# Performance work log

Hardware: AMD Instinct MI355X
Metric: run time of the kernel (lower is better)

The kernel has to match this reference:

```python
import jax, jax.numpy as jnp
import numpy as np

H = W = 64          # input_resolution
C = 256             # dim
HEADS = 8
WS = 8              # window_size
SHIFT = WS // 2
DEPTH = 2           # block 0: no shift, block 1: shifted + mask
HIDDEN = 4 * C      # mlp_ratio * dim
B = 8
N = WS * WS                 # tokens per window
NW = (H // WS) * (W // WS)  # windows per image
EPS = 1e-5


def _rel_pos_index():
    coords = np.stack(np.meshgrid(np.arange(WS), np.arange(WS), indexing='ij')).reshape(2, -1)
    rel = (coords[:, :, None] - coords[:, None, :]).transpose(1, 2, 0)
    rel[:, :, 0] += WS - 1
    rel[:, :, 1] += WS - 1
    rel[:, :, 0] *= 2 * WS - 1
    return rel.sum(-1)  # [N, N] indices into (2*ws-1)^2 table

REL_IDX = jnp.asarray(_rel_pos_index())


def _attn_mask():
    # Swin shift mask: label 3x3 regions, compare window-token labels
    img = np.zeros((H, W))
    slices = (slice(0, -WS), slice(-WS, -SHIFT), slice(-SHIFT, None))
    cnt = 0
    for hs in slices:
        for ws_ in slices:
            img[hs, ws_] = cnt
            cnt += 1
    mw = img.reshape(H // WS, WS, W // WS, WS).transpose(0, 2, 1, 3).reshape(-1, N)
    diff = mw[:, None, :] - mw[:, :, None]
    return jnp.asarray(np.where(diff != 0, -100.0, 0.0), dtype=np.float32)  # [nW, N, N]

ATTN_MASK = _attn_mask()


def layernorm(x, g, b):
    mu = jnp.mean(x, axis=-1, keepdims=True)
    var = jnp.mean((x - mu) ** 2, axis=-1, keepdims=True)
    return (x - mu) * jax.lax.rsqrt(var + EPS) * g + b


def setup_inputs() -> dict:
    key = jax.random.key(0)
    ks = jax.random.split(key, 6)
    s = 0.02
    return {
        'x': jax.random.normal(ks[0], (B, H * W, C), jnp.float32),
        'qkv_w': jax.random.normal(ks[1], (DEPTH, C, 3 * C), jnp.float32) * s,
        'qkv_b': jnp.zeros((DEPTH, 3 * C), jnp.float32),
        'proj_w': jax.random.normal(ks[2], (DEPTH, C, C), jnp.float32) * s,
        'proj_b': jnp.zeros((DEPTH, C), jnp.float32),
        'ln1_g': jnp.ones((DEPTH, C), jnp.float32),
        'ln1_b': jnp.zeros((DEPTH, C), jnp.float32),
        'ln2_g': jnp.ones((DEPTH, C), jnp.float32),
        'ln2_b': jnp.zeros((DEPTH, C), jnp.float32),
        'fc1_w': jax.random.normal(ks[3], (DEPTH, C, HIDDEN), jnp.float32) * s,
        'fc1_b': jnp.zeros((DEPTH, HIDDEN), jnp.float32),
        'fc2_w': jax.random.normal(ks[4], (DEPTH, HIDDEN, C), jnp.float32) * s,
        'fc2_b': jnp.zeros((DEPTH, C), jnp.float32),
        'rpb': jax.random.normal(ks[5], (DEPTH, (2 * WS - 1) ** 2, HEADS), jnp.float32) * s,
    }


def window_attention(xw, qw, qb, pw, pb, rpb_i, mask):
    # xw: [B*nW, N, C]
    B_ = xw.shape[0]
    d = C // HEADS
    qkv = (xw @ qw + qb).reshape(B_, N, 3, HEADS, d).transpose(2, 0, 3, 1, 4)
    q, k, v = qkv[0] * (d ** -0.5), qkv[1], qkv[2]   # [B_, h, N, d]
    attn = jnp.einsum('bhnd,bhmd->bhnm', q, k)
    bias = rpb_i[REL_IDX.reshape(-1)].reshape(N, N, HEADS).transpose(2, 0, 1)
    attn = attn + bias[None]
    if mask is not None:
        attn = attn.reshape(-1, NW, HEADS, N, N) + mask[None, :, None]
        attn = attn.reshape(-1, HEADS, N, N)
    attn = jax.nn.softmax(attn, axis=-1)
    out = jnp.einsum('bhnm,bhmd->bhnd', attn, v).transpose(0, 2, 1, 3).reshape(B_, N, C)
    return out @ pw + pb


def reference(x, qkv_w, qkv_b, proj_w, proj_b, ln1_g, ln1_b, ln2_g, ln2_b,
              fc1_w, fc1_b, fc2_w, fc2_b, rpb):
    for i in range(DEPTH):
        shift = 0 if i % 2 == 0 else SHIFT
        mask = None if shift == 0 else ATTN_MASK
        shortcut = x
        h = layernorm(x, ln1_g[i], ln1_b[i]).reshape(-1, H, W, C)
        if shift:
            h = jnp.roll(h, (-shift, -shift), axis=(1, 2))
        # window partition -> [B*nW, N, C]
        hw = h.reshape(-1, H // WS, WS, W // WS, WS, C).transpose(0, 1, 3, 2, 4, 5).reshape(-1, N, C)
        aw = window_attention(hw, qkv_w[i], qkv_b[i], proj_w[i], proj_b[i], rpb[i], mask)
        # window reverse
        h = aw.reshape(-1, H // WS, W // WS, WS, WS, C).transpose(0, 1, 3, 2, 4, 5).reshape(-1, H, W, C)
        if shift:
            h = jnp.roll(h, (shift, shift), axis=(1, 2))
        x = shortcut + h.reshape(-1, H * W, C)
        m = layernorm(x, ln2_g[i], ln2_b[i])
        m = jax.nn.gelu(m @ fc1_w[i] + fc1_b[i], approximate=False) @ fc2_w[i] + fc2_b[i]
        x = x + m
    return x
```

## Files before the change

### kernel.cpp

```cpp
#include <hip/hip_runtime.h>
#include <hip/hip_bf16.h>


typedef __hip_bfloat16 bf16;
typedef unsigned short u16;
typedef unsigned int u32;
typedef short short8 __attribute__((ext_vector_type(8)));
typedef float floatx4 __attribute__((ext_vector_type(4)));

#define DEVI static __device__ __forceinline__
#define WAITCNT_VM(n) asm volatile("s_waitcnt vmcnt(" #n ")" ::: "memory")

DEVI float lo16(u32 u) { union { u32 i; float f; } x; x.i = u << 16; return x.f; }
DEVI float hi16(u32 u) { union { u32 i; float f; } x; x.i = u & 0xffff0000u; return x.f; }
DEVI float b2f(u16 u) { union { u32 i; float f; } x; x.i = ((u32)u) << 16; return x.f; }
DEVI u16 f2b(float f) {
  union { float f; u32 i; } x; x.f = f;
  u32 r = x.i + 0x7fffu + ((x.i >> 16) & 1u);
  return (u16)(r >> 16);
}
DEVI float in_elem(const void* p, size_t i, int m) {
  return m ? b2f(((const u16*)p)[i]) : ((const float*)p)[i];
}
DEVI int swlab(int g) { return (g < 56) ? 0 : (g < 60 ? 1 : 2); }

DEVI float gelu_cheap(float v) {
  const float u = v * v;
  const float t = v * __builtin_fmaf(0.1029436f, u, 2.3022090f);
  const float e = __builtin_amdgcn_exp2f(t);
  const float r = __builtin_amdgcn_rcpf(e + 1.0f);
  return __builtin_fmaf(-v, r, v);
}

DEVI void async16(const bf16* g, bf16* l) {
  __builtin_amdgcn_global_load_lds((const __attribute__((address_space(1))) u32*)g,
                                   (__attribute__((address_space(3))) u32*)l, 16, 0, 0);
}

__global__ void k_detect(const u32* __restrict__ ln1g, int* __restrict__ mode) {
  if (threadIdx.x == 0 && blockIdx.x == 0)
    *mode = (ln1g[0] == 0x3F803F80u) ? 1 : 0;
}

__global__ __launch_bounds__(256) void k_ingest_ln(const void* __restrict__ xin,
    float* __restrict__ xf, const void* __restrict__ gamw, const void* __restrict__ betw,
    bf16* __restrict__ outp, const int* __restrict__ mode)
{
  const int m = *mode;
  const int l = threadIdx.x & 63, w = threadIdx.x >> 6;
  const int row = blockIdx.x * 4 + w;
  const int t = row & 63, win = row >> 6;
  const int bb = win >> 6, wi = win & 63;
  const int gh = ((wi >> 3) << 3) + (t >> 3);
  const int gw = ((wi & 7) << 3) + (t & 7);
  const int srow = (bb << 12) + (gh << 6) + gw;
  const int cb = l << 2;
  float4 v;
  if (m) {
    const uint2 u = *(const uint2*)((const u16*)xin + (size_t)srow * 256 + cb);
    v = make_float4(lo16(u.x), hi16(u.x), lo16(u.y), hi16(u.y));
  } else {
    v = ((const float4*)((const float*)xin + (size_t)srow * 256))[l];
  }
  ((float4*)(xf + (size_t)srow * 256))[l] = v;
  float s = v.x + v.y + v.z + v.w;
#pragma unroll
  for (int off = 32; off > 0; off >>= 1) s += __shfl_xor(s, off, 64);
  const float mu = s * 0.00390625f;
  const float a = v.x - mu, b = v.y - mu, c = v.z - mu, d = v.w - mu;
  float q = a * a + b * b + c * c + d * d;
#pragma unroll
  for (int off = 32; off > 0; off >>= 1) q += __shfl_xor(q, off, 64);
  const float rs = rsqrtf(q * 0.00390625f + 1e-5f);
  const float o0 = a * rs * in_elem(gamw, cb + 0, m) + in_elem(betw, cb + 0, m);
  const float o1 = b * rs * in_elem(gamw, cb + 1, m) + in_elem(betw, cb + 1, m);
  const float o2 = c * rs * in_elem(gamw, cb + 2, m) + in_elem(betw, cb + 2, m);
  const float o3 = d * rs * in_elem(gamw, cb + 3, m) + in_elem(betw, cb + 3, m);
  const u32 p0 = (u32)f2b(o0) | ((u32)f2b(o1) << 16);
  const u32 p1 = (u32)f2b(o2) | ((u32)f2b(o3) << 16);
  *(uint2*)((u16*)outp + (size_t)row * 256 + cb) = make_uint2(p0, p1);
}

__global__ __launch_bounds__(256) void k_transpose(
    const void* __restrict__ src, bf16* __restrict__ dst,
    const int* __restrict__ mode, int estride, int dstride, int R, int Cn) {
  __shared__ float T[32][33];
  const int m = *mode;
  const int tx = threadIdx.x & 31, ty = threadIdx.x >> 5;
  const int bc = blockIdx.x << 5, br = blockIdx.y << 5;
  for (int d = 0; d < 2; ++d) {
    __syncthreads();
#pragma unroll
    for (int dy = 0; dy < 4; ++dy) {
      const int r = br + ty + dy * 8;
      T[ty + dy * 8][tx] = in_elem(src, (size_t)d * estride + (size_t)r * Cn + bc + tx, m);
    }
    __syncthreads();
#pragma unroll
    for (int dy = 0; dy < 4; ++dy) {
      const int c = bc + ty + dy * 8;
      ((u16*)dst)[(size_t)d * dstride + (size_t)c * R + br + tx] = f2b(T[tx][ty + dy * 8]);
    }
  }
}

template <int EPI>
__global__ __launch_bounds__(256, 3) void k_gemm(
    const bf16* __restrict__ A, const bf16* __restrict__ Bt,
    const void* __restrict__ bias, bf16* __restrict__ outb,
    const int* __restrict__ mode, int boff, int K, int N)
{
  __shared__ __align__(16) bf16 As[3][128 * 32];
  __shared__ __align__(16) bf16 Bs[3][128 * 32];
  __shared__ __align__(16) float EPs[4][4][72];
  const int md = *mode;
  const int tid = threadIdx.x;
  const int l = tid & 63, wid = tid >> 6;
  const int wr = wid >> 1, wc = wid & 1;

  const int gx = gridDim.x;
  const int nwg = gx * gridDim.y;
  int fid = blockIdx.y * gx + blockIdx.x;
  if (!(nwg & 7)) fid = (fid & 7) * (nwg >> 3) + (fid >> 3);
  const int row0 = (fid / gx) * 128;
  const int col0 = (fid % gx) * 128;

  const int lrow = l >> 2;
  const int lkof = (((l & 3) ^ ((l >> 3) & 3)) * 8);
  const int qsw  = (((l >> 4) ^ ((l >> 1) & 3)) * 8);

  floatx4 acc[4][4];
#pragma unroll
  for (int mi = 0; mi < 4; ++mi)
#pragma unroll
    for (int ni = 0; ni < 4; ++ni)
      acc[mi][ni] = (floatx4){0.f, 0.f, 0.f, 0.f};

  auto stage = [&](int b, int kbase) {
    const int kk = kbase + lkof;
#pragma unroll
    for (int c = 0; c < 2; ++c) {
      const int seg = c * 4 + wid;
      async16(A + (size_t)(row0 + seg * 16 + lrow) * K + kk, &As[b][seg * 512]);
      async16(Bt + (size_t)(col0 + seg * 16 + lrow) * K + kk, &Bs[b][seg * 512]);
    }
  };

  const int nsl = K >> 5;
  stage(0, 0);
  stage(1, 32);

  for (int s = 0; s < nsl; ++s) {
    const int cur = s % 3;
    if (s < nsl - 1) { WAITCNT_VM(4); }
    else            { WAITCNT_VM(0); }
    __builtin_amdgcn_s_barrier();
    if (s + 2 < nsl) stage((s + 2) % 3, (s + 2) * 32);

    short8 af[4], bq[4];
#pragma unroll
    for (int mi = 0; mi < 4; ++mi)
      af[mi] = *(const short8*)&As[cur][(wr * 64 + mi * 16 + (l & 15)) * 32 + qsw];
#pragma unroll
    for (int ni = 0; ni < 4; ++ni)
      bq[ni] = *(const short8*)&Bs[cur][(wc * 64 + ni * 16 + (l & 15)) * 32 + qsw];
#pragma unroll
    for (int mi = 0; mi < 4; ++mi)
#pragma unroll
      for (int ni = 0; ni < 4; ++ni)
        acc[mi][ni] = __builtin_amdgcn_mfma_f32_16x16x32_bf16(af[mi], bq[ni], acc[mi][ni], 0, 0, 0);
  }

  float* EPw = &EPs[wid][0][0];
  const int cl = l & 15, rq = l >> 4;
  const int colb = wc * 64 + cl * 4;
  float bias4[4];
#pragma unroll
  for (int i = 0; i < 4; ++i) bias4[i] = in_elem(bias, (size_t)boff + col0 + colb + i, md);

#pragma unroll
  for (int mi = 0; mi < 4; ++mi) {
#pragma unroll
    for (int r = 0; r < 4; ++r) {
#pragma unroll
      for (int ni = 0; ni < 4; ++ni)
        EPw[rq * 72 + ni * 16 + cl] = acc[mi][ni][r];
      const float4 av = *(const float4*)&EPw[rq * 72 + cl * 4];
      float v0 = av.x + bias4[0], v1 = av.y + bias4[1];
      float v2 = av.z + bias4[2], v3 = av.w + bias4[3];
      if (EPI == 1) {
        v0 = gelu_cheap(v0); v1 = gelu_cheap(v1);
        v2 = gelu_cheap(v2); v3 = gelu_cheap(v3);
      }
      const int row = row0 + wr * 64 + mi * 16 + rq * 4 + r;
      const u32 p0 = (u32)f2b(v0) | ((u32)f2b(v1) << 16);
      const u32 p1 = (u32)f2b(v2) | ((u32)f2b(v3) << 16);
      *(uint2*)((u16*)outb + (size_t)row * N + col0 + colb) = make_uint2(p0, p1);
    }
  }
}

template <int MODE>
__global__ __launch_bounds__(256, 2) void k_fullN(
    const bf16* __restrict__ A, const bf16* __restrict__ Bt,
    const void* __restrict__ bias, const void* __restrict__ lng,
    const void* __restrict__ lnb, void* __restrict__ outp,
    float* __restrict__ xf, const int* __restrict__ mode,
    int boff, int lnoff, int K, int shift)
{
  __shared__ __align__(16) char smem[61440];
  bf16* As = (bf16*)smem;
  bf16* Bs = (bf16*)(smem + 12288);
  const int md = *mode;
  const int tid = threadIdx.x;
  const int l = tid & 63, w = tid >> 6;

  int fid = blockIdx.x;
  const int nwg = gridDim.x;
  if (!(nwg & 7)) fid = (fid & 7) * (nwg >> 3) + (fid >> 3);
  const int row0 = fid * 64;

  const int lrow = l >> 2;
  const int lkof = (((l & 3) ^ ((l >> 3) & 3)) * 8);
  const int qsw  = (((l >> 4) ^ ((l >> 1) & 3)) * 8);

  floatx4 acc[16];
#pragma unroll
  for (int ni = 0; ni < 16; ++ni) acc[ni] = (floatx4){0.f, 0.f, 0.f, 0.f};

  auto stage = [&](int b, int kbase) {
    const int kk = kbase + lkof;
    async16(A + (size_t)(row0 + w * 16 + lrow) * K + kk, As + b * 2048 + w * 512);
#pragma unroll
    for (int c = 0; c < 4; ++c) {
      const int seg = c * 4 + w;
      async16(Bt + (size_t)(seg * 16 + lrow) * K + kk, Bs + b * 8192 + seg * 512);
    }
  };

  const int nsl = K >> 5;
  stage(0, 0);
  stage(1, 32);

  for (int s = 0; s < nsl; ++s) {
    const int cur = s % 3;
    if (s < nsl - 1) { WAITCNT_VM(5); }
    else            { WAITCNT_VM(0); }
    __builtin_amdgcn_s_barrier();
    if (s + 2 < nsl) stage((s + 2) % 3, (s + 2) * 32);

    const short8 af = *(const short8*)&As[cur * 2048 + (w * 16 + (l & 15)) * 32 + qsw];
#pragma unroll
    for (int ni = 0; ni < 16; ++ni) {
      const short8 bq = *(const short8*)&Bs[cur * 8192 + (ni * 16 + (l & 15)) * 32 + qsw];
      acc[ni] = __builtin_amdgcn_mfma_f32_16x16x32_bf16(af, bq, acc[ni], 0, 0, 0);
    }
  }

  __syncthreads();

  float* EPw = (float*)smem + w * 1088;
  const int cl = l & 15, rq = l >> 4;
  const int c4 = l * 4;

  float bias4[4], g4[4], b4[4];
#pragma unroll
  for (int i = 0; i < 4; ++i) bias4[i] = in_elem(bias, (size_t)boff + c4 + i, md);
#pragma unroll
  for (int i = 0; i < 4; ++i) {
    g4[i] = in_elem(lng, (size_t)lnoff + c4 + i, md);
    b4[i] = in_elem(lnb, (size_t)lnoff + c4 + i, md);
  }

  for (int r = 0; r < 4; ++r) {
#pragma unroll
    for (int ni = 0; ni < 16; ++ni)
      EPw[rq * 272 + ni * 16 + cl] = acc[ni][r];

#pragma unroll
    for (int g = 0; g < 4; ++g) {
      const int lrow_g = row0 + w * 16 + g * 4 + r;
      const float4 av = *(const float4*)&EPw[g * 272 + c4];

      const int t_ = lrow_g & 63, win = lrow_g >> 6;
      const int bb = win >> 6, wi2 = win & 63;
      int gh = ((wi2 >> 3) << 3) + (t_ >> 3);
      int gw = ((wi2 & 7) << 3) + (t_ & 7);
      gh = (gh + shift) & 63; gw = (gw + shift) & 63;
      const int resrow = (bb << 12) + (gh << 6) + gw;
      const int dstrow = resrow;

      const float4 xv = *(const float4*)(xf + (size_t)resrow * 256 + c4);
      float t0 = av.x + bias4[0] + xv.x;
      float t1 = av.y + bias4[1] + xv.y;
      float t2 = av.z + bias4[2] + xv.z;
      float t3 = av.w + bias4[3] + xv.w;

      float s = t0 + t1 + t2 + t3;
#pragma unroll
      for (int off = 32; off > 0; off >>= 1) s += __shfl_xor(s, off, 64);
      const float mu = s * 0.00390625f;
      const float d0 = t0 - mu, d1 = t1 - mu, d2 = t2 - mu, d3 = t3 - mu;
      float q = d0 * d0 + d1 * d1 + d2 * d2 + d3 * d3;
#pragma unroll
      for (int off = 32; off > 0; off >>= 1) q += __shfl_xor(q, off, 64);
      const float rs = rsqrtf(q * 0.00390625f + 1e-5f);

      *(float4*)(xf + (size_t)resrow * 256 + c4) = make_float4(t0, t1, t2, t3);
      const u32 p0 = (u32)f2b(d0 * rs * g4[0] + b4[0]) | ((u32)f2b(d1 * rs * g4[1] + b4[1]) << 16);
      const u32 p1 = (u32)f2b(d2 * rs * g4[2] + b4[2]) | ((u32)f2b(d3 * rs * g4[3] + b4[3]) << 16);
      *(uint2*)((u16*)outp + (size_t)dstrow * 256 + c4) = make_uint2(p0, p1);
    }
  }
}

template <int MODE>
__global__ __launch_bounds__(512, 2) void k_mlp(
    const bf16* __restrict__ A, const bf16* __restrict__ W1t, const bf16* __restrict__ W2t,
    const void* __restrict__ b1, const void* __restrict__ b2,
    const void* __restrict__ lng, const void* __restrict__ lnb,
    void* __restrict__ outp, float* __restrict__ xf, const int* __restrict__ mode,
    int b1off, int b2off, int lnoff)
{
  __shared__ __align__(16) char smem[163840];
  bf16* Al = (bf16*)smem;
  bf16* Wl = (bf16*)(smem + 65536);
  u16*  Hl = (u16*)(smem + 131072);
  const int md = *mode;
  const int tid = threadIdx.x;
  const int l = tid & 63, w = tid >> 6;
  const int rh = w >> 2, wq = w & 3;
  int fid = blockIdx.x;
  const int nwg = gridDim.x;
  if (!(nwg & 7)) fid = (fid & 7) * (nwg >> 3) + (fid >> 3);
  const int row0 = fid * 128;

  const int lr4 = l >> 2;
  const int lkof = (((l & 3) ^ ((l >> 3) & 3)) * 8);
  const int qsw  = (((l >> 4) ^ ((l >> 1) & 3)) * 8);
  const int cl = l & 15, rq = l >> 4;

  floatx4 acc2[4][4];
#pragma unroll
  for (int mi = 0; mi < 4; ++mi)
#pragma unroll
    for (int ni = 0; ni < 4; ++ni)
      acc2[mi][ni] = (floatx4){0.f, 0.f, 0.f, 0.f};

  auto stageW1 = [&](int c, int s, int b) {
    const size_t gr = (size_t)(c * 128 + w * 16 + lr4) * 256;
#pragma unroll
    for (int ss = 0; ss < 4; ++ss)
      async16(W1t + gr + (s + ss) * 32 + lkof, Wl + b * 16384 + ss * 4096 + w * 512);
  };
  auto stageW2 = [&](int c, int q, int b) {
#pragma unroll
    for (int qq = 0; qq < 2; ++qq)
#pragma unroll
      for (int cc = 0; cc < 2; ++cc) {
        const int seg = w * 2 + cc;
        async16(W2t + (size_t)(seg * 16 + lr4) * 1024 + c * 128 + (q + qq) * 32 + lkof,
                Wl + b * 16384 + qq * 8192 + seg * 512);
      }
  };
  auto stage_g = [&](int g) {
    const int c = g >> 2, sub = g & 3, b = g & 1;
    if (sub < 2) stageW1(c, 4 * sub, b);
    else         stageW2(c, 2 * (sub - 2), b);
  };

#pragma unroll
  for (int s = 0; s < 8; ++s)
    async16(A + (size_t)(row0 + w * 16 + lr4) * 256 + s * 32 + lkof, Al + s * 4096 + w * 512);
  stage_g(0);

  int ph = 0;
  for (int c = 0; c < 8; ++c) {
    floatx4 acc1[4][2];
#pragma unroll
    for (int mi = 0; mi < 4; ++mi)
#pragma unroll
      for (int bni = 0; bni < 2; ++bni)
        acc1[mi][bni] = (floatx4){0.f, 0.f, 0.f, 0.f};

    for (int p = 0; p < 2; ++p, ++ph) {
      WAITCNT_VM(0);
      __builtin_amdgcn_s_barrier();
      if (ph + 1 < 32) stage_g(ph + 1);
      const int buf = ph & 1;
#pragma unroll
      for (int h2 = 0; h2 < 4; ++h2) {
        const int ks = 4 * p + h2;
        short8 af[4];
#pragma unroll
        for (int mi = 0; mi < 4; ++mi)
          af[mi] = *(const short8*)&Al[ks * 4096 + (rh * 64 + mi * 16 + cl) * 32 + qsw];
#pragma unroll
        for (int bni = 0; bni < 2; ++bni) {
          const short8 bq = *(const short8*)(Wl + buf * 16384 + h2 * 4096 +
                                             (wq * 32 + bni * 16 + cl) * 32 + qsw);
#pragma unroll
          for (int mi = 0; mi < 4; ++mi)
            acc1[mi][bni] = __builtin_amdgcn_mfma_f32_16x16x32_bf16(af[mi], bq, acc1[mi][bni], 0, 0, 0);
        }
      }
    }

#pragma unroll
    for (int bni = 0; bni < 2; ++bni) {
      const int h32 = bni * 16 + cl;
      const float bv = in_elem(b1, (size_t)b1off + c * 128 + wq * 32 + h32, md);
      const int hq = h32 >> 3, he = h32 & 7;
#pragma unroll
      for (int mi = 0; mi < 4; ++mi)
#pragma unroll
        for (int r = 0; r < 4; ++r) {
          const int hr = rh * 64 + mi * 16 + rq * 4 + r;
          Hl[wq * 4096 + hr * 32 + ((hq ^ ((hr >> 1) & 3)) * 8) + he] =
              f2b(gelu_cheap(acc1[mi][bni][r] + bv));
        }
    }
    asm volatile("s_waitcnt lgkmcnt(0)" ::: "memory");

    for (int p = 0; p < 2; ++p, ++ph) {
      WAITCNT_VM(0);
      __builtin_amdgcn_s_barrier();
      if (ph + 1 < 32) stage_g(ph + 1);
      const int buf = ph & 1;
#pragma unroll
      for (int qq = 0; qq < 2; ++qq) {
        const int q2 = 2 * p + qq;
        short8 hf[4];
#pragma unroll
        for (int mi = 0; mi < 4; ++mi)
          hf[mi] = *(const short8*)((const bf16*)&Hl[q2 * 4096 + (rh * 64 + mi * 16 + cl) * 32 + qsw]);
#pragma unroll
        for (int ni = 0; ni < 4; ++ni) {
          const short8 bq = *(const short8*)(Wl + buf * 16384 + qq * 8192 +
                                             (wq * 64 + ni * 16 + cl) * 32 + qsw);
#pragma unroll
          for (int mi = 0; mi < 4; ++mi)
            acc2[mi][ni] = __builtin_amdgcn_mfma_f32_16x16x32_bf16(hf[mi], bq, acc2[mi][ni], 0, 0, 0);
        }
      }
    }
  }

  __syncthreads();
  float* EPf = (float*)smem;
#pragma unroll
  for (int mi = 0; mi < 4; ++mi)
#pragma unroll
    for (int ni = 0; ni < 4; ++ni)
#pragma unroll
      for (int r = 0; r < 4; ++r)
        EPf[(rh * 64 + mi * 16 + rq * 4 + r) * 272 + wq * 64 + ni * 16 + cl] = acc2[mi][ni][r];
  __syncthreads();

  const int c4 = l * 4;
  float bias4[4], g4[4], b4[4];
#pragma unroll
  for (int i = 0; i < 4; ++i) bias4[i] = in_elem(b2, (size_t)b2off + c4 + i, md);
  if (MODE == 1) {
#pragma unroll
    for (int i = 0; i < 4; ++i) {
      g4[i] = in_elem(lng, (size_t)lnoff + c4 + i, md);
      b4[i] = in_elem(lnb, (size_t)lnoff + c4 + i, md);
    }
  }

  for (int rr = 0; rr < 16; ++rr) {
    const int lrow_g = row0 + w * 16 + rr;
    const float4 av = *(const float4*)&EPf[(w * 16 + rr) * 272 + c4];
    const float4 xv = *(const float4*)(xf + (size_t)lrow_g * 256 + c4);
    float t0 = av.x + bias4[0] + xv.x;
    float t1 = av.y + bias4[1] + xv.y;
    float t2 = av.z + bias4[2] + xv.z;
    float t3 = av.w + bias4[3] + xv.w;

    if (MODE == 2) {
      *(float4*)((float*)outp + (size_t)lrow_g * 256 + c4) = make_float4(t0, t1, t2, t3);
      continue;
    }

    const int bb = lrow_g >> 12, th = (lrow_g >> 6) & 63, tw = lrow_g & 63;
    const int gh = (th + 60) & 63, gw = (tw + 60) & 63;
    const int wi2 = ((gh >> 3) << 3) + (gw >> 3);
    const int tt = ((gh & 7) << 3) + (gw & 7);
    const int dstrow = (bb << 12) + (wi2 << 6) + tt;

    float s = t0 + t1 + t2 + t3;
#pragma unroll
    for (int off = 32; off > 0; off >>= 1) s += __shfl_xor(s, off, 64);
    const float mu = s * 0.00390625f;
    const float d0 = t0 - mu, d1 = t1 - mu, d2 = t2 - mu, d3 = t3 - mu;
    float q = d0 * d0 + d1 * d1 + d2 * d2 + d3 * d3;
#pragma unroll
    for (int off = 32; off > 0; off >>= 1) q += __shfl_xor(q, off, 64);
    const float rs = rsqrtf(q * 0.00390625f + 1e-5f);

    *(float4*)(xf + (size_t)lrow_g * 256 + c4) = make_float4(t0, t1, t2, t3);
    const u32 p0 = (u32)f2b(d0 * rs * g4[0] + b4[0]) | ((u32)f2b(d1 * rs * g4[1] + b4[1]) << 16);
    const u32 p1 = (u32)f2b(d2 * rs * g4[2] + b4[2]) | ((u32)f2b(d3 * rs * g4[3] + b4[3]) << 16);
    *(uint2*)((u16*)outp + (size_t)dstrow * 256 + c4) = make_uint2(p0, p1);
  }
}

__global__ __launch_bounds__(256, 2) void k_attn(
    const bf16* __restrict__ qkv, const void* __restrict__ rpb,
    bf16* __restrict__ outp, const int* __restrict__ mode, int eoff, int shifted)
{
  __shared__ __align__(16) u16 Pl[4][64][72];
  __shared__ __align__(16) u16 Vt[4][32][72];
  __shared__ float rpbs[4][228];
  const int md = *mode;
  const int l = threadIdx.x & 63, w = threadIdx.x >> 6;
  const int cl = l & 15, qd = l >> 4;
  const int ko = qd * 8;
  const int win = blockIdx.x;
  const int wi = win & 63;
  const int whb = (wi >> 3) << 3, wwb = (wi & 7) << 3;
  const size_t rowbase = (size_t)win * 64 * 768;

  for (int hh = 0; hh < 2; ++hh) {
    const int h = w + hh * 4;
    for (int i = l; i < 225; i += 64)
      rpbs[w][i] = in_elem(rpb, (size_t)eoff + (size_t)i * 8 + h, md);
    {
      const u16* vrow = (const u16*)(qkv + rowbase + (size_t)l * 768 + 512 + h * 32);
#pragma unroll
      for (int n = 0; n < 32; ++n) Vt[w][n][l] = vrow[n];
    }
    short8 qf[4], kf[4];
#pragma unroll
    for (int t = 0; t < 4; ++t) {
      qf[t] = *(const short8*)(qkv + rowbase + (size_t)(t * 16 + cl) * 768 + h * 32 + ko);
      kf[t] = *(const short8*)(qkv + rowbase + (size_t)(t * 16 + cl) * 768 + 256 + h * 32 + ko);
    }
    __syncthreads();

    floatx4 S[4][4];
#pragma unroll
    for (int mi = 0; mi < 4; ++mi)
#pragma unroll
      for (int ni = 0; ni < 4; ++ni)
        S[mi][ni] = __builtin_amdgcn_mfma_f32_16x16x32_bf16(qf[mi], kf[ni], (floatx4){0.f, 0.f, 0.f, 0.f}, 0, 0, 0);

    int cty[4], ctx[4], clab[4];
#pragma unroll
    for (int ni = 0; ni < 4; ++ni) {
      const int ct = ni * 16 + cl;
      cty[ni] = ct >> 3; ctx[ni] = ct & 7;
      clab[ni] = shifted ? (swlab(whb + cty[ni]) * 3 + swlab(wwb + ctx[ni])) : 0;
    }

    float invs[4][4];
#pragma unroll
    for (int mi = 0; mi < 4; ++mi) {
#pragma unroll
      for (int r = 0; r < 4; ++r) {
        const int rt = mi * 16 + qd * 4 + r;
        const int rty = rt >> 3, rtx = rt & 7;
        const int rlab = shifted ? (swlab(whb + rty) * 3 + swlab(wwb + rtx)) : 0;
        float sv[4];
#pragma unroll
        for (int ni = 0; ni < 4; ++ni) {
          float x = S[mi][ni][r] * 0.17677669529663687f;
          x += rpbs[w][(rty - cty[ni] + 7) * 15 + (rtx - ctx[ni] + 7)];
          if (shifted && (rlab != clab[ni])) x -= 100.f;
          sv[ni] = x;
        }
        float mx = fmaxf(fmaxf(sv[0], sv[1]), fmaxf(sv[2], sv[3]));
        mx = fmaxf(mx, __shfl_xor(mx, 1, 64));
        mx = fmaxf(mx, __shfl_xor(mx, 2, 64));
        mx = fmaxf(mx, __shfl_xor(mx, 4, 64));
        mx = fmaxf(mx, __shfl_xor(mx, 8, 64));
        float sum = 0.f;
#pragma unroll
        for (int ni = 0; ni < 4; ++ni) { sv[ni] = __expf(sv[ni] - mx); sum += sv[ni]; }
        sum += __shfl_xor(sum, 1, 64);
        sum += __shfl_xor(sum, 2, 64);
        sum += __shfl_xor(sum, 4, 64);
        sum += __shfl_xor(sum, 8, 64);
        invs[mi][r] = __builtin_amdgcn_rcpf(sum);
#pragma unroll
        for (int ni = 0; ni < 4; ++ni) Pl[w][rt][ni * 16 + cl] = f2b(sv[ni]);
      }
    }
    __syncthreads();

    floatx4 O[4][2];
#pragma unroll
    for (int mi = 0; mi < 4; ++mi)
#pragma unroll
      for (int nv = 0; nv < 2; ++nv)
        O[mi][nv] = (floatx4){0.f, 0.f, 0.f, 0.f};
    short8 vf[2][2];
#pragma unroll
    for (int nv = 0; nv < 2; ++nv)
#pragma unroll
      for (int kk = 0; kk < 2; ++kk)
        vf[nv][kk] = *(const short8*)&Vt[w][nv * 16 + cl][kk * 32 + ko];
#pragma unroll
    for (int mi = 0; mi < 4; ++mi) {
      const short8 pf0 = *(const short8*)&Pl[w][mi * 16 + cl][ko];
      const short8 pf1 = *(const short8*)&Pl[w][mi * 16 + cl][32 + ko];
#pragma unroll
      for (int nv = 0; nv < 2; ++nv) {
        O[mi][nv] = __builtin_amdgcn_mfma_f32_16x16x32_bf16(pf0, vf[nv][0], O[mi][nv], 0, 0, 0);
        O[mi][nv] = __builtin_amdgcn_mfma_f32_16x16x32_bf16(pf1, vf[nv][1], O[mi][nv], 0, 0, 0);
      }
    }

#pragma unroll
    for (int mi = 0; mi < 4; ++mi)
#pragma unroll
      for (int nv = 0; nv < 2; ++nv)
#pragma unroll
        for (int r = 0; r < 4; ++r) {
          const int row = mi * 16 + qd * 4 + r;
          ((u16*)outp)[((size_t)win * 64 + row) * 256 + h * 32 + nv * 16 + cl] =
              f2b(O[mi][nv][r] * invs[mi][r]);
        }
    __syncthreads();
  }
}

extern "C" void kernel_launch(void* const* d_in, const int* in_sizes, int n_in,
                              void* d_out, int out_size, void* d_ws, size_t ws_size,
                              hipStream_t stream) {
  (void)in_sizes; (void)n_in; (void)out_size; (void)ws_size;
  const void* x_in   = d_in[0];
  const void* qkv_w  = d_in[1];
  const void* qkv_b  = d_in[2];
  const void* proj_w = d_in[3];
  const void* proj_b = d_in[4];
  const void* ln1_g  = d_in[5];
  const void* ln1_b  = d_in[6];
  const void* ln2_g  = d_in[7];
  const void* ln2_b  = d_in[8];
  const void* fc1_w  = d_in[9];
  const void* fc1_b  = d_in[10];
  const void* fc2_w  = d_in[11];
  const void* fc2_b  = d_in[12];
  const void* rpb    = d_in[13];

  char* ws = (char*)d_ws;
  float* xf  = (float*)ws;
  bf16* bufQ = (bf16*)(ws + 100663296);
  bf16* bufB = (bf16*)(ws + 150994944);
  bf16* wT   = (bf16*)(ws + 167772160);
  int* mode  = (int*)(ws + 170917888);

  k_detect<<<1, 1, 0, stream>>>((const u32*)ln1_g, mode);
  k_ingest_ln<<<8192, 256, 0, stream>>>(x_in, xf, ln1_g, ln1_b, bufB, mode);

  k_transpose<<<dim3(24, 8), 256, 0, stream>>>(qkv_w,  wT,          mode, 196608, 786432, 256, 768);
  k_transpose<<<dim3(8, 8), 256, 0, stream>>>(proj_w, wT + 196608, mode, 65536, 786432, 256, 256);
  k_transpose<<<dim3(32, 8), 256, 0, stream>>>(fc1_w, wT + 262144, mode, 262144, 786432, 256, 1024);
  k_transpose<<<dim3(8, 32), 256, 0, stream>>>(fc2_w, wT + 524288, mode, 262144, 786432, 1024, 256);

  for (int i = 0; i < 2; ++i) {
    const int shift = i ? 4 : 0;
    bf16* base  = wT + (size_t)i * 786432;
    bf16* qkvT  = base;
    bf16* projT = base + 196608;
    bf16* fc1T  = base + 262144;
    bf16* fc2T  = base + 524288;

    k_gemm<0><<<dim3(6, 256), 256, 0, stream>>>(bufB, qkvT, qkv_b, bufQ, mode, i * 768, 256, 768);
    k_attn<<<512, 256, 0, stream>>>(bufQ, rpb, bufB, mode, i * 1800, i);
    k_fullN<0><<<512, 256, 0, stream>>>(bufB, projT, proj_b, ln2_g, ln2_b, bufQ, xf, mode,
                                        i * 256, i * 256, 256, shift);
    if (i == 0)
      k_mlp<1><<<256, 512, 0, stream>>>(bufQ, fc1T, fc2T, fc1_b, fc2_b, ln1_g, ln1_b,
                                        bufB, xf, mode, 0, 0, 256);
    else
      k_mlp<2><<<256, 512, 0, stream>>>(bufQ, fc1T, fc2T, fc1_b, fc2_b, nullptr, nullptr,
                                        d_out, xf, mode, 1024, 256, 0);
  }
}
```

Before: 388.8 us.

## Precompute bias+mask table, vectorize V staging, drop per-wave barriers in attention

```diff
diff --git a/kernel.cpp b/kernel.cpp
--- a/kernel.cpp
+++ b/kernel.cpp
@@ -22,7 +22,6 @@
 DEVI float in_elem(const void* p, size_t i, int m) {
   return m ? b2f(((const u16*)p)[i]) : ((const float*)p)[i];
 }
-DEVI int swlab(int g) { return (g < 56) ? 0 : (g < 60 ? 1 : 2); }
 
 DEVI float gelu_cheap(float v) {
   const float u = v * v;
@@ -40,6 +39,25 @@
 __global__ void k_detect(const u32* __restrict__ ln1g, int* __restrict__ mode) {
   if (threadIdx.x == 0 && blockIdx.x == 0)
     *mode = (ln1g[0] == 0x3F803F80u) ? 1 : 0;
+}
+
+__global__ void k_bias(const void* __restrict__ rpb, float* __restrict__ bt,
+                       const int* __restrict__ mode) {
+  const int m = *mode;
+  const int idx = blockIdx.x * 256 + threadIdx.x;
+  const int ct = idx & 63, rt = (idx >> 6) & 63, h = (idx >> 12) & 7;
+  const int ty = (idx >> 15) & 3, d = idx >> 17;
+  const int rty = rt >> 3, rtx = rt & 7, cty = ct >> 3, ctx = ct & 7;
+  const int rel = (rty - cty + 7) * 15 + (rtx - ctx + 7);
+  float v = in_elem(rpb, (size_t)d * 1800 + (size_t)rel * 8 + h, m);
+  if (d) {
+    const int rlr = (ty >> 1) ? ((rty < 4) ? 1 : 2) : 0;
+    const int rlc = (ty & 1) ? ((rtx < 4) ? 1 : 2) : 0;
+    const int clr = (ty >> 1) ? ((cty < 4) ? 1 : 2) : 0;
+    const int clc = (ty & 1) ? ((ctx < 4) ? 1 : 2) : 0;
+    if (rlr != clr || rlc != clc) v -= 100.f;
+  }
+  bt[idx] = v;
 }
 
 __global__ __launch_bounds__(256) void k_ingest_ln(const void* __restrict__ xin,
@@ -507,29 +525,33 @@
 }
 
 __global__ __launch_bounds__(256, 2) void k_attn(
-    const bf16* __restrict__ qkv, const void* __restrict__ rpb,
-    bf16* __restrict__ outp, const int* __restrict__ mode, int eoff, int shifted)
+    const bf16* __restrict__ qkv, const float* __restrict__ bT,
+    bf16* __restrict__ outp, int d, int shifted)
 {
   __shared__ __align__(16) u16 Pl[4][64][72];
   __shared__ __align__(16) u16 Vt[4][32][72];
-  __shared__ float rpbs[4][228];
-  const int md = *mode;
   const int l = threadIdx.x & 63, w = threadIdx.x >> 6;
   const int cl = l & 15, qd = l >> 4;
   const int ko = qd * 8;
   const int win = blockIdx.x;
   const int wi = win & 63;
-  const int whb = (wi >> 3) << 3, wwb = (wi & 7) << 3;
+  const int type = shifted ? ((((wi >> 3) == 7) ? 2 : 0) + (((wi & 7) == 7) ? 1 : 0)) : 0;
+  const float* btb = bT + (((size_t)d * 4 + type) * 8) * 4096;
   const size_t rowbase = (size_t)win * 64 * 768;
 
   for (int hh = 0; hh < 2; ++hh) {
     const int h = w + hh * 4;
-    for (int i = l; i < 225; i += 64)
-      rpbs[w][i] = in_elem(rpb, (size_t)eoff + (size_t)i * 8 + h, md);
+    const float* bth = btb + (size_t)h * 4096;
     {
       const u16* vrow = (const u16*)(qkv + rowbase + (size_t)l * 768 + 512 + h * 32);
-#pragma unroll
-      for (int n = 0; n < 32; ++n) Vt[w][n][l] = vrow[n];
+      short8 vv[4];
+#pragma unroll
+      for (int j = 0; j < 4; ++j) vv[j] = *(const short8*)(vrow + j * 8);
+#pragma unroll
+      for (int j = 0; j < 4; ++j)
+#pragma unroll
+        for (int e = 0; e < 8; ++e)
+          Vt[w][j * 8 + e][l] = (u16)vv[j][e];
     }
     short8 qf[4], kf[4];
 #pragma unroll
@@ -537,7 +559,6 @@
       qf[t] = *(const short8*)(qkv + rowbase + (size_t)(t * 16 + cl) * 768 + h * 32 + ko);
       kf[t] = *(const short8*)(qkv + rowbase + (size_t)(t * 16 + cl) * 768 + 256 + h * 32 + ko);
     }
-    __syncthreads();
 
     floatx4 S[4][4];
 #pragma unroll
@@ -546,30 +567,17 @@
       for (int ni = 0; ni < 4; ++ni)
         S[mi][ni] = __builtin_amdgcn_mfma_f32_16x16x32_bf16(qf[mi], kf[ni], (floatx4){0.f, 0.f, 0.f, 0.f}, 0, 0, 0);
 
-    int cty[4], ctx[4], clab[4];
-#pragma unroll
-    for (int ni = 0; ni < 4; ++ni) {
-      const int ct = ni * 16 + cl;
-      cty[ni] = ct >> 3; ctx[ni] = ct & 7;
-      clab[ni] = shifted ? (swlab(whb + cty[ni]) * 3 + swlab(wwb + ctx[ni])) : 0;
-    }
-
     float invs[4][4];
 #pragma unroll
     for (int mi = 0; mi < 4; ++mi) {
 #pragma unroll
       for (int r = 0; r < 4; ++r) {
         const int rt = mi * 16 + qd * 4 + r;
-        const int rty = rt >> 3, rtx = rt & 7;
-        const int rlab = shifted ? (swlab(whb + rty) * 3 + swlab(wwb + rtx)) : 0;
+        const float* bR = bth + rt * 64 + cl;
         float sv[4];
 #pragma unroll
-        for (int ni = 0; ni < 4; ++ni) {
-          float x = S[mi][ni][r] * 0.17677669529663687f;
-          x += rpbs[w][(rty - cty[ni] + 7) * 15 + (rtx - ctx[ni] + 7)];
-          if (shifted && (rlab != clab[ni])) x -= 100.f;
-          sv[ni] = x;
-        }
+        for (int ni = 0; ni < 4; ++ni)
+          sv[ni] = __builtin_fmaf(S[mi][ni][r], 0.17677669529663687f, bR[ni * 16]);
         float mx = fmaxf(fmaxf(sv[0], sv[1]), fmaxf(sv[2], sv[3]));
         mx = fmaxf(mx, __shfl_xor(mx, 1, 64));
         mx = fmaxf(mx, __shfl_xor(mx, 2, 64));
@@ -587,7 +595,6 @@
         for (int ni = 0; ni < 4; ++ni) Pl[w][rt][ni * 16 + cl] = f2b(sv[ni]);
       }
     }
-    __syncthreads();
 
     floatx4 O[4][2];
 #pragma unroll
@@ -622,7 +629,6 @@
           ((u16*)outp)[((size_t)win * 64 + row) * 256 + h * 32 + nv * 16 + cl] =
               f2b(O[mi][nv][r] * invs[mi][r]);
         }
-    __syncthreads();
   }
 }
 
@@ -646,13 +652,15 @@
   const void* rpb    = d_in[13];
 
   char* ws = (char*)d_ws;
-  float* xf  = (float*)ws;
-  bf16* bufQ = (bf16*)(ws + 100663296);
-  bf16* bufB = (bf16*)(ws + 150994944);
-  bf16* wT   = (bf16*)(ws + 167772160);
-  int* mode  = (int*)(ws + 170917888);
+  float* xf    = (float*)ws;
+  bf16* bufQ  = (bf16*)(ws + 100663296);
+  bf16* bufB  = (bf16*)(ws + 150994944);
+  bf16* wT    = (bf16*)(ws + 167772160);
+  int* mode   = (int*)(ws + 170917888);
+  float* biasT = (float*)(ws + 171966464);
 
   k_detect<<<1, 1, 0, stream>>>((const u32*)ln1_g, mode);
+  k_bias<<<1024, 256, 0, stream>>>(rpb, biasT, mode);
   k_ingest_ln<<<8192, 256, 0, stream>>>(x_in, xf, ln1_g, ln1_b, bufB, mode);
 
   k_transpose<<<dim3(24, 8), 256, 0, stream>>>(qkv_w,  wT,          mode, 196608, 786432, 256, 768);
@@ -669,7 +677,7 @@
     bf16* fc2T  = base + 524288;
 
     k_gemm<0><<<dim3(6, 256), 256, 0, stream>>>(bufB, qkvT, qkv_b, bufQ, mode, i * 768, 256, 768);
-    k_attn<<<512, 256, 0, stream>>>(bufQ, rpb, bufB, mode, i * 1800, i);
+    k_attn<<<512, 256, 0, stream>>>(bufQ, biasT, bufB, i, i);
     k_fullN<0><<<512, 256, 0, stream>>>(bufB, projT, proj_b, ln2_g, ln2_b, bufQ, xf, mode,
                                         i * 256, i * 256, 256, shift);
     if (i == 0)
```

After: 391.8 us. Within noise of the previous version (+0.8%).
